# Performance work log

Hardware: AMD Instinct MI355X
Metric: run time of the kernel (lower is better)

## Reference

```python
import jax, jax.numpy as jnp
import numpy as np

NGROUP, CIN, COUT, K, HIDDEN = 8, 16, 16, 5, True


def _build_mask():
    # Group-causal PixelCNN-style mask for a 5x5 kernel.
    # Spatial: rows above center fully visible; center row visible left of center.
    # Center tap: input group g_in visible to output group g_out iff
    #   g_in <= g_out (hidden layer) or g_in < g_out (input layer).
    nout, cinall = NGROUP * COUT, NGROUP * CIN
    c = K // 2
    m = np.zeros((nout, cinall, K, K), dtype=np.float32)
    m[:, :, :c, :] = 1.0          # rows strictly above center
    m[:, :, c, :c] = 1.0          # center row, left of center
    g_out = np.arange(nout)[:, None] // COUT   # (nout,1)
    g_in = np.arange(cinall)[None, :] // CIN   # (1,cinall)
    center_ok = (g_in <= g_out) if HIDDEN else (g_in < g_out)
    m[:, :, c, c] = center_ok.astype(np.float32)
    return jnp.asarray(m)

_MASK = _build_mask()


def setup_inputs() -> dict:
    key = jax.random.key(0)
    k1, k2 = jax.random.split(key)
    x = jax.random.normal(k1, (8, 128, 256, 512), dtype=jnp.float32)
    weight = jax.random.uniform(k2, (128, 128, 5, 5), dtype=jnp.float32)
    bias = jnp.zeros((128,), dtype=jnp.float32)
    slope = jnp.zeros((128,), dtype=jnp.float32)  # PReLU slope (zero -> ReLU)
    return {"x": x, "weight": weight, "bias": bias, "slope": slope}


def reference(x, weight, bias, slope):
    w = weight * _MASK  # apply causal group mask
    # context pad by 2 then valid 5x5 conv == SAME padding conv
    y = jax.lax.conv_general_dilated(
        x, w, window_strides=(1, 1), padding=((2, 2), (2, 2)),
        dimension_numbers=("NCHW", "OIHW", "NCHW"))
    y = y + bias[None, :, None, None]
    a = slope[None, :, None, None]
    return jnp.where(y > 0, y, a * y)  # per-channel PReLU
```

## Files before the change

kernel.cpp:

```cpp
#include <hip/hip_runtime.h>
#include <hip/hip_bf16.h>

typedef __attribute__((ext_vector_type(8))) short short8;
typedef __attribute__((ext_vector_type(4))) float f32x4;

#define CH 128
#define H 256
#define W 512
#define PH 258
#define PW 516
#define NTAPS 13
#define P_BYTES (PH * PW * CH * 2)
#define P_SHORTS (PH * PW * CH)
#define CHW (CH * H * W)

#define GRAN_PER_ROW 544
#define NLOADS 52
#define BUF_SHORTS (3328 * 8)
#define ROW_SHORTS (GRAN_PER_ROW * 8)

#define GLD_LDS16(g, l)                                                        \
  __builtin_amdgcn_global_load_lds(                                            \
      (const __attribute__((address_space(1))) void*)(g),                      \
      (__attribute__((address_space(3))) void*)(l), 16, 0, 0)

__global__ void zero_pads(unsigned int* __restrict__ Pd) {
    int row  = blockIdx.x;
    int slab = blockIdx.y;
    unsigned int* base = Pd + (size_t)slab * (P_SHORTS / 2);
    int tid = threadIdx.x;
    if (row < 2) {
        unsigned int* r = base + (size_t)row * (PW * 64);
        for (int i = tid; i < PW * 64; i += 256) r[i] = 0u;
    } else {
        int seg = tid >> 6;
        int col = seg < 2 ? seg : 512 + seg;
        base[((size_t)row * PW + col) * 64 + (tid & 63)] = 0u;
    }
}

__global__ void premask_weights(const float* __restrict__ w,
                                __hip_bfloat16* __restrict__ Wt2) {
    int idx  = blockIdx.x * 256 + threadIdx.x;
    int frag = idx >> 9;
    int r    = idx & 511;
    int l    = r >> 3;
    int e    = r & 7;
    int t    = frag >> 5;
    int ob   = (frag >> 2) & 7;
    int kcg  = frag & 3;
    int oc   = ob * 16 + (l & 15);
    int ic   = kcg * 32 + (l >> 4) * 8 + e;
    int ky   = t < 5 ? 0 : (t < 10 ? 1 : 2);
    int kx   = t - ky * 5;
    float v  = w[(oc * CH + ic) * 25 + ky * 5 + kx];
    if (t == 12 && ((ic >> 4) > (oc >> 4))) v = 0.f;
    Wt2[idx] = __float2bfloat16(v);
}

__global__ void transpose_pad_all(const float* __restrict__ x,
                                  __hip_bfloat16* __restrict__ Pbase) {
    __shared__ float tile[32][33];
    const float* xn = x + (size_t)blockIdx.z * CHW;
    unsigned short* P = (unsigned short*)(Pbase + (size_t)blockIdx.z * P_SHORTS);
    int h  = blockIdx.y;
    int wt = blockIdx.x & 15;
    int ct = blockIdx.x >> 4;
    int tx = threadIdx.x & 31;
    int ty = threadIdx.x >> 5;
#pragma unroll
    for (int r = 0; r < 4; ++r) {
        int c = ct * 32 + ty + r * 8;
        tile[ty + r * 8][tx] = xn[(c * H + h) * W + wt * 32 + tx];
    }
    __syncthreads();
    int wl = threadIdx.x >> 3;
    int cq = threadIdx.x & 7;
    union { ushort4 u; __hip_bfloat16 hh[4]; } v;
    v.hh[0] = __float2bfloat16(tile[cq * 4 + 0][wl]);
    v.hh[1] = __float2bfloat16(tile[cq * 4 + 1][wl]);
    v.hh[2] = __float2bfloat16(tile[cq * 4 + 2][wl]);
    v.hh[3] = __float2bfloat16(tile[cq * 4 + 3][wl]);
    *reinterpret_cast<ushort4*>(
        P + ((size_t)(h + 2) * PW + (wt * 32 + wl + 2)) * CH + ct * 32 + cq * 4) = v.u;
}

__global__ __launch_bounds__(512, 2)
void conv_mfma_all(const __hip_bfloat16* __restrict__ Pbase,
                   const __hip_bfloat16* __restrict__ Wt2,
                   const float* __restrict__ bias,
                   const float* __restrict__ slope,
                   float* __restrict__ out) {
    __shared__ short lds[2 * BUF_SHORTS];
    int d   = blockIdx.x;
    int lid = (d & 7) * 256 + (d >> 3);
    int bz  = lid >> 8;
    int by  = (lid >> 2) & 63;
    int bx  = lid & 3;
    const __hip_bfloat16* P = Pbase + (size_t)bz * P_SHORTS;
    float* outn = out + (size_t)bz * CHW;
    int h0    = by << 2;
    int w0    = bx << 7;
    int tid   = threadIdx.x;
    int lane  = tid & 63;
    int wv    = tid >> 6;
    int l15   = lane & 15;
    int khi   = lane >> 4;
    int obf   = (wv & 1) * 4;
    int hsel  = wv >> 1;

    f32x4 acc[4][8];
#pragma unroll
    for (int mi = 0; mi < 4; ++mi)
#pragma unroll
        for (int ni = 0; ni < 8; ++ni)
            acc[mi][ni] = (f32x4){0.f, 0.f, 0.f, 0.f};

    const short* Wt2s = (const short*)Wt2;

    int stoff[7];
#pragma unroll
    for (int i = 0; i < 7; ++i) {
        int s    = wv + i * 8;
        int g64  = (s << 6) + lane;
        int row  = (g64 >= 544) + (g64 >= 1088) + (g64 >= 1632) +
                   (g64 >= 2176) + (g64 >= 2720) + (g64 >= 3264);
        int rowc = row < 6 ? row : 5;
        int G    = g64 - row * GRAN_PER_ROW;
        int pair = G >> 3;
        int qd   = (G & 7) ^ (pair & 7);
        int px   = pair * 2 + (qd >> 2);
        int chk  = qd & 3;
        int pxc  = px < 132 ? px : 131;
        stoff[i] = ((h0 + rowc) * PW + (w0 + pxc)) * CH + chk * 8;
    }
    int bq[5];
#pragma unroll
    for (int kx = 0; kx < 5; ++kx) {
        int pxb  = kx + l15;
        int pair = pxb >> 1;
        bq[kx] = ((pair << 3) + ((((pxb & 1) << 2) | khi) ^ (pair & 7))) << 3;
    }

    auto stage = [&](int kk, int bsel) {
#pragma unroll
        for (int i = 0; i < 7; ++i) {
            int s = wv + i * 8;
            if (s < NLOADS)
                GLD_LDS16(P + stoff[i] + kk * 32,
                          (char*)lds + bsel * (BUF_SHORTS * 2) + (s << 10));
        }
    };

    stage(0, 0);
    __syncthreads();

    for (int kk = 0; kk < 4; ++kk) {
        const int cur = kk & 1;
        if (kk < 3) stage(kk + 1, cur ^ 1);

        const short* apb = Wt2s + ((obf * 4 + kk) << 9) + (lane << 3);
        const short* bb  = lds + cur * BUF_SHORTS + hsel * ROW_SHORTS;
#pragma unroll
        for (int t = 0; t < NTAPS; ++t) {
            int ky  = t < 5 ? 0 : (t < 10 ? 1 : 2);
            int kx  = t - ky * 5;
            const short* ap = apb + t * 16384;
            const short* bp = bb + ky * ROW_SHORTS + bq[kx];
            short8 a[4], b[8];
#pragma unroll
            for (int mi = 0; mi < 4; ++mi)
                a[mi] = *reinterpret_cast<const short8*>(ap + mi * 2048);
#pragma unroll
            for (int ni = 0; ni < 8; ++ni)
                b[ni] = *reinterpret_cast<const short8*>(bp + ni * 512);
            __builtin_amdgcn_s_setprio(1);
#pragma unroll
            for (int mi = 0; mi < 4; ++mi)
#pragma unroll
                for (int ni = 0; ni < 8; ++ni)
                    acc[mi][ni] = __builtin_amdgcn_mfma_f32_16x16x32_bf16(
                        a[mi], b[ni], acc[mi][ni], 0, 0, 0);
            __builtin_amdgcn_s_setprio(0);
        }
        __syncthreads();
    }

    int hrow = h0 + hsel;
#pragma unroll
    for (int mi = 0; mi < 4; ++mi) {
        int ocb = obf * 16 + mi * 16 + 4 * khi;
        f32x4 b4 = *reinterpret_cast<const f32x4*>(bias + ocb);
        f32x4 s4 = *reinterpret_cast<const f32x4*>(slope + ocb);
#pragma unroll
        for (int i = 0; i < 4; ++i) {
            float* orow = outn + ((ocb + i) * H + hrow) * W + w0;
#pragma unroll
            for (int ni = 0; ni < 8; ++ni) {
                float v = acc[mi][ni][i] + b4[i];
                v = v > 0.f ? v : s4[i] * v;
                orow[ni * 16 + l15] = v;
            }
        }
    }
}

extern "C" void kernel_launch(void* const* d_in, const int* in_sizes, int n_in,
                              void* d_out, int out_size, void* d_ws, size_t ws_size,
                              hipStream_t stream) {
    const float* x      = (const float*)d_in[0];
    const float* weight = (const float*)d_in[1];
    const float* bias   = (const float*)d_in[2];
    const float* slope  = (const float*)d_in[3];
    float* out = (float*)d_out;

    __hip_bfloat16* Pbase = (__hip_bfloat16*)d_ws;
    __hip_bfloat16* Wt2   = (__hip_bfloat16*)((char*)d_ws + 8 * (size_t)P_BYTES);

    zero_pads<<<dim3(PH, 8), 256, 0, stream>>>((unsigned int*)d_ws);
    premask_weights<<<832, 256, 0, stream>>>(weight, Wt2);
    transpose_pad_all<<<dim3(64, 256, 8), 256, 0, stream>>>(x, Pbase);
    conv_mfma_all<<<2048, 512, 0, stream>>>(Pbase, Wt2, bias, slope, out);
}
```

Before: 573.3 us.

## Switch conv MFMA tiling from 16x16x32 to 32x32x16 bf16 instructions

Replaces the per-wave 4x8 grid of 16x16x32 MFMAs with a 2x4 grid of 32x32x16 MFMAs, each split into two K-halves. The weight prepack layout, the LDS B-fragment addressing and the epilogue output mapping are all rewritten to match the 32-lane fragment shape. The aim is fewer LDS and global fragment loads per FLOP and higher MFMA throughput per issued instruction. The trade-offs are different accumulator register use and LDS access patterns that could cause bank conflicts.

```diff
diff --git a/kernel.cpp b/kernel.cpp
--- a/kernel.cpp
+++ b/kernel.cpp
@@ -3,6 +3,7 @@
 
 typedef __attribute__((ext_vector_type(8))) short short8;
 typedef __attribute__((ext_vector_type(4))) float f32x4;
+typedef __attribute__((ext_vector_type(16))) float f32x16;
 
 #define CH 128
 #define H 256
@@ -40,22 +41,23 @@
 }
 
 __global__ void premask_weights(const float* __restrict__ w,
-                                __hip_bfloat16* __restrict__ Wt2) {
+                                __hip_bfloat16* __restrict__ Wt3) {
     int idx  = blockIdx.x * 256 + threadIdx.x;
     int frag = idx >> 9;
     int r    = idx & 511;
     int l    = r >> 3;
     int e    = r & 7;
     int t    = frag >> 5;
-    int ob   = (frag >> 2) & 7;
-    int kcg  = frag & 3;
-    int oc   = ob * 16 + (l & 15);
-    int ic   = kcg * 32 + (l >> 4) * 8 + e;
+    int mib  = (frag >> 3) & 3;
+    int kk   = (frag >> 1) & 3;
+    int ks   = frag & 1;
+    int oc   = mib * 32 + (l & 31);
+    int ic   = kk * 32 + ks * 16 + (l >> 5) * 8 + e;
     int ky   = t < 5 ? 0 : (t < 10 ? 1 : 2);
     int kx   = t - ky * 5;
     float v  = w[(oc * CH + ic) * 25 + ky * 5 + kx];
     if (t == 12 && ((ic >> 4) > (oc >> 4))) v = 0.f;
-    Wt2[idx] = __float2bfloat16(v);
+    Wt3[idx] = __float2bfloat16(v);
 }
 
 __global__ void transpose_pad_all(const float* __restrict__ x,
@@ -87,7 +89,7 @@
 
 __global__ __launch_bounds__(512, 2)
 void conv_mfma_all(const __hip_bfloat16* __restrict__ Pbase,
-                   const __hip_bfloat16* __restrict__ Wt2,
+                   const __hip_bfloat16* __restrict__ Wt3,
                    const float* __restrict__ bias,
                    const float* __restrict__ slope,
                    float* __restrict__ out) {
@@ -104,19 +106,19 @@
     int tid   = threadIdx.x;
     int lane  = tid & 63;
     int wv    = tid >> 6;
-    int l15   = lane & 15;
-    int khi   = lane >> 4;
-    int obf   = (wv & 1) * 4;
+    int l31   = lane & 31;
+    int lhi   = lane >> 5;
+    int ohf   = wv & 1;
     int hsel  = wv >> 1;
 
-    f32x4 acc[4][8];
-#pragma unroll
-    for (int mi = 0; mi < 4; ++mi)
-#pragma unroll
-        for (int ni = 0; ni < 8; ++ni)
-            acc[mi][ni] = (f32x4){0.f, 0.f, 0.f, 0.f};
-
-    const short* Wt2s = (const short*)Wt2;
+    f32x16 acc[2][4];
+#pragma unroll
+    for (int mi = 0; mi < 2; ++mi)
+#pragma unroll
+        for (int ni = 0; ni < 4; ++ni)
+            acc[mi][ni] = (f32x16){0.f};
+
+    const short* Wt3s = (const short*)Wt3;
 
     int stoff[7];
 #pragma unroll
@@ -134,12 +136,15 @@
         int pxc  = px < 132 ? px : 131;
         stoff[i] = ((h0 + rowc) * PW + (w0 + pxc)) * CH + chk * 8;
     }
-    int bq[5];
+    int bqk[5][2];
 #pragma unroll
     for (int kx = 0; kx < 5; ++kx) {
-        int pxb  = kx + l15;
+        int pxb  = kx + l31;
         int pair = pxb >> 1;
-        bq[kx] = ((pair << 3) + ((((pxb & 1) << 2) | khi) ^ (pair & 7))) << 3;
+#pragma unroll
+        for (int ks = 0; ks < 2; ++ks)
+            bqk[kx][ks] =
+                ((pair << 3) + ((((pxb & 1) << 2) | (ks * 2 + lhi)) ^ (pair & 7))) << 3;
     }
 
     auto stage = [&](int kk, int bsel) {
@@ -159,28 +164,36 @@
         const int cur = kk & 1;
         if (kk < 3) stage(kk + 1, cur ^ 1);
 
-        const short* apb = Wt2s + ((obf * 4 + kk) << 9) + (lane << 3);
+        const short* apb = Wt3s + ohf * 8192 + kk * 1024 + (lane << 3);
         const short* bb  = lds + cur * BUF_SHORTS + hsel * ROW_SHORTS;
 #pragma unroll
         for (int t = 0; t < NTAPS; ++t) {
             int ky  = t < 5 ? 0 : (t < 10 ? 1 : 2);
             int kx  = t - ky * 5;
             const short* ap = apb + t * 16384;
-            const short* bp = bb + ky * ROW_SHORTS + bq[kx];
-            short8 a[4], b[8];
-#pragma unroll
-            for (int mi = 0; mi < 4; ++mi)
-                a[mi] = *reinterpret_cast<const short8*>(ap + mi * 2048);
-#pragma unroll
-            for (int ni = 0; ni < 8; ++ni)
-                b[ni] = *reinterpret_cast<const short8*>(bp + ni * 512);
+            const short* bp = bb + ky * ROW_SHORTS;
+            short8 a[2][2], b[4][2];
+#pragma unroll
+            for (int mi = 0; mi < 2; ++mi)
+#pragma unroll
+                for (int ks = 0; ks < 2; ++ks)
+                    a[mi][ks] = *reinterpret_cast<const short8*>(
+                        ap + mi * 4096 + ks * 512);
+#pragma unroll
+            for (int ni = 0; ni < 4; ++ni)
+#pragma unroll
+                for (int ks = 0; ks < 2; ++ks)
+                    b[ni][ks] = *reinterpret_cast<const short8*>(
+                        bp + bqk[kx][ks] + ni * 1024);
             __builtin_amdgcn_s_setprio(1);
 #pragma unroll
-            for (int mi = 0; mi < 4; ++mi)
-#pragma unroll
-                for (int ni = 0; ni < 8; ++ni)
-                    acc[mi][ni] = __builtin_amdgcn_mfma_f32_16x16x32_bf16(
-                        a[mi], b[ni], acc[mi][ni], 0, 0, 0);
+            for (int mi = 0; mi < 2; ++mi)
+#pragma unroll
+                for (int ni = 0; ni < 4; ++ni)
+#pragma unroll
+                    for (int ks = 0; ks < 2; ++ks)
+                        acc[mi][ni] = __builtin_amdgcn_mfma_f32_32x32x16_bf16(
+                            a[mi][ks], b[ni][ks], acc[mi][ni], 0, 0, 0);
             __builtin_amdgcn_s_setprio(0);
         }
         __syncthreads();
@@ -188,18 +201,21 @@
 
     int hrow = h0 + hsel;
 #pragma unroll
-    for (int mi = 0; mi < 4; ++mi) {
-        int ocb = obf * 16 + mi * 16 + 4 * khi;
-        f32x4 b4 = *reinterpret_cast<const f32x4*>(bias + ocb);
-        f32x4 s4 = *reinterpret_cast<const f32x4*>(slope + ocb);
-#pragma unroll
-        for (int i = 0; i < 4; ++i) {
-            float* orow = outn + ((ocb + i) * H + hrow) * W + w0;
-#pragma unroll
-            for (int ni = 0; ni < 8; ++ni) {
-                float v = acc[mi][ni][i] + b4[i];
-                v = v > 0.f ? v : s4[i] * v;
-                orow[ni * 16 + l15] = v;
+    for (int mi = 0; mi < 2; ++mi) {
+#pragma unroll
+        for (int q = 0; q < 4; ++q) {
+            int oc0 = ohf * 64 + mi * 32 + q * 8 + 4 * lhi;
+            f32x4 b4 = *reinterpret_cast<const f32x4*>(bias + oc0);
+            f32x4 s4 = *reinterpret_cast<const f32x4*>(slope + oc0);
+#pragma unroll
+            for (int j = 0; j < 4; ++j) {
+                float* orow = outn + ((oc0 + j) * H + hrow) * W + w0;
+#pragma unroll
+                for (int ni = 0; ni < 4; ++ni) {
+                    float v = acc[mi][ni][q * 4 + j] + b4[j];
+                    v = v > 0.f ? v : s4[j] * v;
+                    orow[ni * 32 + l31] = v;
+                }
             }
         }
     }
@@ -215,10 +231,10 @@
     float* out = (float*)d_out;
 
     __hip_bfloat16* Pbase = (__hip_bfloat16*)d_ws;
-    __hip_bfloat16* Wt2   = (__hip_bfloat16*)((char*)d_ws + 8 * (size_t)P_BYTES);
+    __hip_bfloat16* Wt3   = (__hip_bfloat16*)((char*)d_ws + 8 * (size_t)P_BYTES);
 
     zero_pads<<<dim3(PH, 8), 256, 0, stream>>>((unsigned int*)d_ws);
-    premask_weights<<<832, 256, 0, stream>>>(weight, Wt2);
+    premask_weights<<<832, 256, 0, stream>>>(weight, Wt3);
     transpose_pad_all<<<dim3(64, 256, 8), 256, 0, stream>>>(x, Pbase);
-    conv_mfma_all<<<2048, 512, 0, stream>>>(Pbase, Wt2, bias, slope, out);
-}
+    conv_mfma_all<<<2048, 512, 0, stream>>>(Pbase, Wt3, bias, slope, out);
+}
```

Result: slower. 630.3 us (+9.9%).

## Retile conv waves to two output rows and reuse B fragments across ky

Applied to the files above, without the earlier changes.

Each wave previously covered one output row by 128 pixels by 64 output channels. It now covers two output rows by 64 pixels by 64 channels. The loop is reordered to kx outer and ky inner, so LDS B fragments loaded for one input row are shared by the two output rows that need them. This cuts LDS read traffic per MFMA by roughly a third. In exchange it holds up to four rows of B fragments live, which raises VGPR pressure under the 512x2 launch bound and risks spills or lower occupancy.

```diff
diff --git a/kernel.cpp b/kernel.cpp
--- a/kernel.cpp
+++ b/kernel.cpp
@@ -106,15 +106,18 @@
     int wv    = tid >> 6;
     int l15   = lane & 15;
     int khi   = lane >> 4;
-    int obf   = (wv & 1) * 4;
-    int hsel  = wv >> 1;
-
-    f32x4 acc[4][8];
+    int ohf   = wv & 1;
+    int hp    = (wv >> 1) & 1;
+    int pxh   = wv >> 2;
+
+    f32x4 acc[4][2][4];
 #pragma unroll
     for (int mi = 0; mi < 4; ++mi)
 #pragma unroll
-        for (int ni = 0; ni < 8; ++ni)
-            acc[mi][ni] = (f32x4){0.f, 0.f, 0.f, 0.f};
+        for (int o = 0; o < 2; ++o)
+#pragma unroll
+            for (int ni = 0; ni < 4; ++ni)
+                acc[mi][o][ni] = (f32x4){0.f, 0.f, 0.f, 0.f};
 
     const short* Wt2s = (const short*)Wt2;
 
@@ -137,7 +140,7 @@
     int bq[5];
 #pragma unroll
     for (int kx = 0; kx < 5; ++kx) {
-        int pxb  = kx + l15;
+        int pxb  = pxh * 64 + kx + l15;
         int pair = pxb >> 1;
         bq[kx] = ((pair << 3) + ((((pxb & 1) << 2) | khi) ^ (pair & 7))) << 3;
     }
@@ -159,47 +162,65 @@
         const int cur = kk & 1;
         if (kk < 3) stage(kk + 1, cur ^ 1);
 
-        const short* apb = Wt2s + ((obf * 4 + kk) << 9) + (lane << 3);
-        const short* bb  = lds + cur * BUF_SHORTS + hsel * ROW_SHORTS;
-#pragma unroll
-        for (int t = 0; t < NTAPS; ++t) {
-            int ky  = t < 5 ? 0 : (t < 10 ? 1 : 2);
-            int kx  = t - ky * 5;
-            const short* ap = apb + t * 16384;
-            const short* bp = bb + ky * ROW_SHORTS + bq[kx];
-            short8 a[4], b[8];
-#pragma unroll
-            for (int mi = 0; mi < 4; ++mi)
-                a[mi] = *reinterpret_cast<const short8*>(ap + mi * 2048);
-#pragma unroll
-            for (int ni = 0; ni < 8; ++ni)
-                b[ni] = *reinterpret_cast<const short8*>(bp + ni * 512);
-            __builtin_amdgcn_s_setprio(1);
-#pragma unroll
-            for (int mi = 0; mi < 4; ++mi)
-#pragma unroll
-                for (int ni = 0; ni < 8; ++ni)
-                    acc[mi][ni] = __builtin_amdgcn_mfma_f32_16x16x32_bf16(
-                        a[mi], b[ni], acc[mi][ni], 0, 0, 0);
-            __builtin_amdgcn_s_setprio(0);
+        const short* apb = Wt2s + ((ohf * 16 + kk) << 9) + (lane << 3);
+        const short* bb  = lds + cur * BUF_SHORTS + (hp * 2) * ROW_SHORTS;
+#pragma unroll
+        for (int kx = 0; kx < 5; ++kx) {
+            const int nky = (kx < 3) ? 3 : 2;
+            short8 B[4][4];
+#pragma unroll
+            for (int ni = 0; ni < 4; ++ni) {
+                B[0][ni] = *reinterpret_cast<const short8*>(
+                    bb + 0 * ROW_SHORTS + bq[kx] + ni * 512);
+                B[1][ni] = *reinterpret_cast<const short8*>(
+                    bb + 1 * ROW_SHORTS + bq[kx] + ni * 512);
+            }
+#pragma unroll
+            for (int ky = 0; ky < 3; ++ky) {
+                if (ky >= nky) break;
+                if (ky + 2 <= nky) {
+#pragma unroll
+                    for (int ni = 0; ni < 4; ++ni)
+                        B[ky + 2][ni] = *reinterpret_cast<const short8*>(
+                            bb + (ky + 2) * ROW_SHORTS + bq[kx] + ni * 512);
+                }
+                const short* ap = apb + (ky * 5 + kx) * 16384;
+                short8 a[4];
+#pragma unroll
+                for (int mi = 0; mi < 4; ++mi)
+                    a[mi] = *reinterpret_cast<const short8*>(ap + mi * 2048);
+                __builtin_amdgcn_s_setprio(1);
+#pragma unroll
+                for (int mi = 0; mi < 4; ++mi)
+#pragma unroll
+                    for (int o = 0; o < 2; ++o)
+#pragma unroll
+                        for (int ni = 0; ni < 4; ++ni)
+                            acc[mi][o][ni] = __builtin_amdgcn_mfma_f32_16x16x32_bf16(
+                                a[mi], B[ky + o][ni], acc[mi][o][ni], 0, 0, 0);
+                __builtin_amdgcn_s_setprio(0);
+            }
         }
         __syncthreads();
     }
 
-    int hrow = h0 + hsel;
 #pragma unroll
     for (int mi = 0; mi < 4; ++mi) {
-        int ocb = obf * 16 + mi * 16 + 4 * khi;
+        int ocb = ohf * 64 + mi * 16 + 4 * khi;
         f32x4 b4 = *reinterpret_cast<const f32x4*>(bias + ocb);
         f32x4 s4 = *reinterpret_cast<const f32x4*>(slope + ocb);
 #pragma unroll
-        for (int i = 0; i < 4; ++i) {
-            float* orow = outn + ((ocb + i) * H + hrow) * W + w0;
-#pragma unroll
-            for (int ni = 0; ni < 8; ++ni) {
-                float v = acc[mi][ni][i] + b4[i];
-                v = v > 0.f ? v : s4[i] * v;
-                orow[ni * 16 + l15] = v;
+        for (int o = 0; o < 2; ++o) {
+            int hrow = h0 + hp * 2 + o;
+#pragma unroll
+            for (int i = 0; i < 4; ++i) {
+                float* orow = outn + ((ocb + i) * H + hrow) * W + w0 + pxh * 64;
+#pragma unroll
+                for (int ni = 0; ni < 4; ++ni) {
+                    float v = acc[mi][o][ni][i] + b4[i];
+                    v = v > 0.f ? v : s4[i] * v;
+                    orow[ni * 16 + l15] = v;
+                }
             }
         }
     }
```

Result: no change. 568.8 us (-0.8%).
